# Kernel tuning notes

Measured on AMD Instinct MI355X. Metric: run time of the kernel, lower is better.

The kernel has to match this reference:

```python
import jax, jax.numpy as jnp
import numpy as np
import math

B, L, C, H = 8, 1024, 1024, 8
EPS = 1e-5

def setup_inputs() -> dict:
    key = jax.random.key(0)
    ks = jax.random.split(key, 5)
    s = 0.02
    return {
        "x": jax.random.normal(ks[0], (B, L, C), dtype=jnp.float32),
        "ln_g": jnp.ones((C,), dtype=jnp.float32),
        "ln_b": jnp.zeros((C,), dtype=jnp.float32),
        "w_qkv": jax.random.normal(ks[1], (C, 3 * C), dtype=jnp.float32) * s,
        "b_qkv": jax.random.normal(ks[2], (3 * C,), dtype=jnp.float32) * s,
        "w_out": jax.random.normal(ks[3], (C, C), dtype=jnp.float32) * s,
        "b_out": jax.random.normal(ks[4], (C,), dtype=jnp.float32) * s,
    }

def reference(x, ln_g, ln_b, w_qkv, b_qkv, w_out, b_out):
    bs, length, width = x.shape
    ch = width // H
    # LayerNorm over channels
    mu = jnp.mean(x, axis=-1, keepdims=True)
    var = jnp.mean(jnp.square(x - mu), axis=-1, keepdims=True)
    xn = (x - mu) * jax.lax.rsqrt(var + EPS) * ln_g + ln_b
    # fused QKV projection
    qkv = jnp.einsum('blc,cd->bld', xn, w_qkv) + b_qkv  # [B, L, 3C]
    q, k, v = jnp.split(qkv, 3, axis=2)                 # each [B, L, C]
    scale = 1.0 / math.sqrt(math.sqrt(ch))
    # faithful raw row-major reshape as in the torch .view call
    q = (q * scale).reshape(bs * H, length, ch)
    k = (k * scale).reshape(bs * H, length, ch)
    v = v.reshape(bs * H, length, ch)
    w = jnp.einsum('bqc,bkc->bqk', q, k)                # [B*H, L, L] score matrix
    w = jax.nn.softmax(w.astype(jnp.float32), axis=-1).astype(q.dtype)
    attn = jnp.einsum('bqk,bkc->bqc', w, v).reshape(bs, length, -1)
    out = jnp.einsum('blc,cd->bld', attn, w_out) + b_out + xn  # residual uses normalized x
    return out
```

## Files before the change

### kernel.cpp

```cpp
#include <hip/hip_runtime.h>
#include <hip/hip_bf16.h>


typedef __attribute__((ext_vector_type(8))) short short8;
typedef __attribute__((ext_vector_type(4))) float f32x4;

#define QK_SCALE 0.29730177875068026f

__device__ __forceinline__ float bf2f(ushort u) {
    union { float f; unsigned int i; } c; c.i = ((unsigned int)u) << 16; return c.f;
}
__device__ __forceinline__ ushort f2bf(float f) {
    union { float f; unsigned int i; } c; c.f = f;
    unsigned int x = c.i;
    return (ushort)((x + 0x7FFFu + ((x >> 16) & 1u)) >> 16);
}

__device__ __forceinline__ void gload_lds16(const ushort* g, ushort* l) {
    __builtin_amdgcn_global_load_lds(
        (const __attribute__((address_space(1))) unsigned int*)g,
        (__attribute__((address_space(3))) unsigned int*)l, 16, 0, 0);
}

__global__ __launch_bounds__(256) void prep_kernel(
    const float* __restrict__ x, const float* __restrict__ g,
    const float* __restrict__ b, ushort* __restrict__ xn,
    const float* __restrict__ w_qkv, ushort* __restrict__ wqkvT,
    const float* __restrict__ w_out, ushort* __restrict__ woutT) {
    __shared__ ushort t[32][33];
    int bid = blockIdx.x;
    int tid = threadIdx.x;
    if (bid < 2048) {
        int w = tid >> 6, lane = tid & 63;
        int row = bid * 4 + w;
        const float* xr = x + (size_t)row * 1024;
        float v[4][4];
        float s1 = 0.f, s2 = 0.f;
#pragma unroll
        for (int j = 0; j < 4; j++) {
            float4 t4 = *(const float4*)(xr + lane * 4 + j * 256);
            v[j][0] = t4.x; v[j][1] = t4.y; v[j][2] = t4.z; v[j][3] = t4.w;
#pragma unroll
            for (int e = 0; e < 4; e++) { s1 += v[j][e]; s2 += v[j][e] * v[j][e]; }
        }
#pragma unroll
        for (int m = 32; m >= 1; m >>= 1) { s1 += __shfl_xor(s1, m); s2 += __shfl_xor(s2, m); }
        float mu = s1 * (1.0f / 1024.0f);
        float var = s2 * (1.0f / 1024.0f) - mu * mu;
        float rs = rsqrtf(var + 1e-5f);
#pragma unroll
        for (int j = 0; j < 4; j++) {
            int c0 = lane * 4 + j * 256;
            float4 gg = *(const float4*)(g + c0);
            float4 bb = *(const float4*)(b + c0);
            float gA[4] = {gg.x, gg.y, gg.z, gg.w};
            float bA[4] = {bb.x, bb.y, bb.z, bb.w};
            ushort o[4];
#pragma unroll
            for (int e = 0; e < 4; e++) o[e] = f2bf((v[j][e] - mu) * rs * gA[e] + bA[e]);
            uint2 pk;
            pk.x = (uint)o[0] | ((uint)o[1] << 16);
            pk.y = (uint)o[2] | ((uint)o[3] << 16);
            *(uint2*)(xn + (size_t)row * 1024 + c0) = pk;
        }
    } else {
        const float* in; ushort* out; int R, Cc, bx, by;
        if (bid < 5120) {
            int tt = bid - 2048;
            in = w_qkv; out = wqkvT; R = 1024; Cc = 3072;
            bx = (tt % 96) * 32; by = (tt / 96) * 32;
        } else {
            int tt = bid - 5120;
            in = w_out; out = woutT; R = 1024; Cc = 1024;
            bx = (tt % 32) * 32; by = (tt / 32) * 32;
        }
        int tx = tid & 31, ty = tid >> 5;
#pragma unroll
        for (int j = 0; j < 32; j += 8)
            t[ty + j][tx] = f2bf(in[(size_t)(by + ty + j) * Cc + bx + tx]);
        __syncthreads();
#pragma unroll
        for (int j = 0; j < 32; j += 8)
            out[(size_t)(bx + ty + j) * R + by + tx] = t[tx][ty + j];
    }
}

__device__ __forceinline__ void stage8(const ushort* __restrict__ Ab,
                                       const ushort* __restrict__ Bb, int t2,
                                       ushort* AsD, ushort* BsD, int tid) {
    const ushort* As_src = Ab + t2 * 64;
    const ushort* Bs_src = Bb + t2 * 64;
#pragma unroll
    for (int i = 0; i < 4; i++) {
        int lin = i * 256 + tid;
        int r = lin >> 3, p = lin & 7;
        int l = p ^ (r & 7);
        gload_lds16(As_src + (size_t)r * 1024 + l * 8, &AsD[lin * 8]);
    }
#pragma unroll
    for (int i = 0; i < 4; i++) {
        int lin = i * 256 + tid;
        int r = lin >> 3, p = lin & 7;
        int l = p ^ (r & 7);
        gload_lds16(Bs_src + (size_t)r * 1024 + l * 8, &BsD[lin * 8]);
    }
}

__global__ __launch_bounds__(256, 2) void gemm_qkv(
    const ushort* __restrict__ A, const ushort* __restrict__ Bt,
    const float* __restrict__ bias, ushort* __restrict__ out0,
    ushort* __restrict__ out1, ushort* __restrict__ wv) {
    __shared__ __align__(16) ushort As[2][128 * 64];
    __shared__ __align__(16) ushort Bs[2][128 * 64];

    int tid = threadIdx.x;
    int lane = tid & 63, w = tid >> 6;
    int l15 = lane & 15, q4 = lane >> 4;
    int wrM = (w >> 1) * 64;
    int wcN = (w & 1) * 64;

    int bid = blockIdx.x;
    int xcd = bid & 7;
    int i = bid >> 3;
    int by = xcd * 8 + (i & 7);
    int bx = i >> 3;
    int rowBase = by * 128, colBase = bx * 128;

    const ushort* Ab = A + (size_t)rowBase * 1024;
    const ushort* Bb = Bt + (size_t)colBase * 1024;

    f32x4 acc[4][4];
    f32x4 zero = {0.f, 0.f, 0.f, 0.f};
#pragma unroll
    for (int mi = 0; mi < 4; mi++)
#pragma unroll
        for (int ni = 0; ni < 4; ni++) acc[mi][ni] = zero;

    stage8(Ab, Bb, 0, &As[0][0], &Bs[0][0], tid);
    stage8(Ab, Bb, 1, &As[1][0], &Bs[1][0], tid);
    asm volatile("s_waitcnt vmcnt(8)" ::: "memory");
    __builtin_amdgcn_s_barrier();

    for (int t = 0; t < 16; ++t) {
        const int cur = t & 1;
        const ushort* Ac = &As[cur][0];
        const ushort* Bc = &Bs[cur][0];

        short8 aF[4][2], bF[4][2];
#pragma unroll
        for (int kk = 0; kk < 2; kk++) {
#pragma unroll
            for (int mi = 0; mi < 4; mi++) {
                int r = wrM + mi * 16 + l15;
                aF[mi][kk] = *(const short8*)&Ac[r * 64 + ((kk * 4 + q4) ^ (r & 7)) * 8];
            }
#pragma unroll
            for (int ni = 0; ni < 4; ni++) {
                int r = wcN + ni * 16 + l15;
                bF[ni][kk] = *(const short8*)&Bc[r * 64 + ((kk * 4 + q4) ^ (r & 7)) * 8];
            }
        }

        __builtin_amdgcn_s_setprio(1);
#pragma unroll
        for (int mi = 0; mi < 4; mi++)
#pragma unroll
            for (int ni = 0; ni < 4; ni++)
                acc[mi][ni] = __builtin_amdgcn_mfma_f32_16x16x32_bf16(
                    aF[mi][0], bF[ni][0], acc[mi][ni], 0, 0, 0);
        __builtin_amdgcn_s_setprio(0);

        asm volatile("s_waitcnt lgkmcnt(0)" ::: "memory");
        __builtin_amdgcn_s_barrier();
        if (t < 14) stage8(Ab, Bb, t + 2, &As[cur][0], &Bs[cur][0], tid);

        __builtin_amdgcn_s_setprio(1);
#pragma unroll
        for (int mi = 0; mi < 4; mi++)
#pragma unroll
            for (int ni = 0; ni < 4; ni++)
                acc[mi][ni] = __builtin_amdgcn_mfma_f32_16x16x32_bf16(
                    aF[mi][1], bF[ni][1], acc[mi][ni], 0, 0, 0);
        __builtin_amdgcn_s_setprio(0);

        if (t < 15) {
            if (t < 14) asm volatile("s_waitcnt vmcnt(8)" ::: "memory");
            else        asm volatile("s_waitcnt vmcnt(0)" ::: "memory");
            __builtin_amdgcn_s_barrier();
        }
    }

    if (colBase < 2048) {
#pragma unroll
        for (int ni = 0; ni < 4; ni++) {
            int col = colBase + wcN + ni * 16 + l15;
            float bv = bias[col];
            int cc = col & 1023;
            ushort* dst = (col < 1024) ? out0 : out1;
#pragma unroll
            for (int mi = 0; mi < 4; mi++) {
                f32x4 a = acc[mi][ni];
#pragma unroll
                for (int r = 0; r < 4; r++) {
                    int row = rowBase + wrM + mi * 16 + q4 * 4 + r;
                    dst[(size_t)row * 1024 + cc] = f2bf((a[r] + bv) * QK_SCALE);
                }
            }
        }
    } else {
        int g = rowBase >> 7;
        int s7 = (colBase - 2048) >> 7;
        ushort* Wg = wv + (size_t)g * 131072 + (size_t)s7 * 128;
#pragma unroll
        for (int ni = 0; ni < 4; ni++) {
            int col = colBase + wcN + ni * 16 + l15;
            float bv = bias[col];
            int d = wcN + ni * 16 + l15;
#pragma unroll
            for (int mi = 0; mi < 4; mi++) {
                f32x4 a = acc[mi][ni];
                int off0 = wrM + mi * 16 + q4 * 4;
                ushort o0 = f2bf(a[0] + bv), o1 = f2bf(a[1] + bv);
                ushort o2 = f2bf(a[2] + bv), o3 = f2bf(a[3] + bv);
                uint2 pk;
                pk.x = (uint)o0 | ((uint)o1 << 16);
                pk.y = (uint)o2 | ((uint)o3 << 16);
                *(uint2*)&Wg[(size_t)d * 1024 + off0] = pk;
            }
        }
    }
}

__global__ __launch_bounds__(256, 2) void gemm_out(
    const ushort* __restrict__ A, const ushort* __restrict__ Bt,
    const float* __restrict__ bias, const ushort* __restrict__ resid,
    float* __restrict__ outf) {
    __shared__ __align__(16) ushort As[2][128 * 64];
    __shared__ __align__(16) ushort Bs[2][128 * 64];

    int tid = threadIdx.x;
    int lane = tid & 63, w = tid >> 6;
    int l15 = lane & 15, q4 = lane >> 4;
    int wrM = (w >> 1) * 64;
    int wcN = (w & 1) * 64;

    int bid = blockIdx.x;
    int xcd = bid & 7;
    int i = bid >> 3;
    int by = xcd * 8 + (i & 7);
    int bx = i >> 3;
    int rowBase = by * 128, colBase = bx * 128;

    const ushort* Ab = A + (size_t)rowBase * 1024;
    const ushort* Bb = Bt + (size_t)colBase * 1024;

    f32x4 acc[4][4];
    f32x4 zero = {0.f, 0.f, 0.f, 0.f};
#pragma unroll
    for (int mi = 0; mi < 4; mi++)
#pragma unroll
        for (int ni = 0; ni < 4; ni++) acc[mi][ni] = zero;

    stage8(Ab, Bb, 0, &As[0][0], &Bs[0][0], tid);
    stage8(Ab, Bb, 1, &As[1][0], &Bs[1][0], tid);
    asm volatile("s_waitcnt vmcnt(8)" ::: "memory");
    __builtin_amdgcn_s_barrier();

    for (int t = 0; t < 16; ++t) {
        const int cur = t & 1;
        const ushort* Ac = &As[cur][0];
        const ushort* Bc = &Bs[cur][0];

        short8 aF[4][2], bF[4][2];
#pragma unroll
        for (int kk = 0; kk < 2; kk++) {
#pragma unroll
            for (int mi = 0; mi < 4; mi++) {
                int r = wrM + mi * 16 + l15;
                aF[mi][kk] = *(const short8*)&Ac[r * 64 + ((kk * 4 + q4) ^ (r & 7)) * 8];
            }
#pragma unroll
            for (int ni = 0; ni < 4; ni++) {
                int r = wcN + ni * 16 + l15;
                bF[ni][kk] = *(const short8*)&Bc[r * 64 + ((kk * 4 + q4) ^ (r & 7)) * 8];
            }
        }

        __builtin_amdgcn_s_setprio(1);
#pragma unroll
        for (int mi = 0; mi < 4; mi++)
#pragma unroll
            for (int ni = 0; ni < 4; ni++)
                acc[mi][ni] = __builtin_amdgcn_mfma_f32_16x16x32_bf16(
                    aF[mi][0], bF[ni][0], acc[mi][ni], 0, 0, 0);
        __builtin_amdgcn_s_setprio(0);

        asm volatile("s_waitcnt lgkmcnt(0)" ::: "memory");
        __builtin_amdgcn_s_barrier();
        if (t < 14) stage8(Ab, Bb, t + 2, &As[cur][0], &Bs[cur][0], tid);

        __builtin_amdgcn_s_setprio(1);
#pragma unroll
        for (int mi = 0; mi < 4; mi++)
#pragma unroll
            for (int ni = 0; ni < 4; ni++)
                acc[mi][ni] = __builtin_amdgcn_mfma_f32_16x16x32_bf16(
                    aF[mi][1], bF[ni][1], acc[mi][ni], 0, 0, 0);
        __builtin_amdgcn_s_setprio(0);

        if (t < 15) {
            if (t < 14) asm volatile("s_waitcnt vmcnt(8)" ::: "memory");
            else        asm volatile("s_waitcnt vmcnt(0)" ::: "memory");
            __builtin_amdgcn_s_barrier();
        }
    }

#pragma unroll
    for (int ni = 0; ni < 4; ni++) {
        int col = colBase + wcN + ni * 16 + l15;
        float bv = bias[col];
#pragma unroll
        for (int mi = 0; mi < 4; mi++) {
            f32x4 a = acc[mi][ni];
#pragma unroll
            for (int r = 0; r < 4; r++) {
                int row = rowBase + wrM + mi * 16 + q4 * 4 + r;
                outf[(size_t)row * 1024 + col] =
                    a[r] + bv + bf2f(resid[(size_t)row * 1024 + col]);
            }
        }
    }
}

__device__ __forceinline__ void attn_stage(const ushort* __restrict__ Kh,
                                           const ushort* __restrict__ Wg,
                                           int kt, ushort* KsD, ushort* VtD,
                                           int tid) {
#pragma unroll
    for (int i = 0; i < 4; i++) {
        int linear = i * 512 + tid;
        int r = linear >> 4, p = linear & 15;
        int l = p ^ (r & 15);
        gload_lds16(&Kh[(size_t)(kt * 128 + r) * 128 + l * 8], &KsD[linear * 8]);
    }
#pragma unroll
    for (int i = 0; i < 4; i++) {
        int linear = i * 512 + tid;
        int d = linear >> 4, p = linear & 15;
        int half = p >> 3, pl = p & 7;
        int cl = pl ^ (d & 7);
        gload_lds16(&Wg[(size_t)d * 1024 + cl * 128 + kt * 16 + half * 8],
                    &VtD[linear * 8]);
    }
}

__global__ __launch_bounds__(512) void attn_kernel(
    const ushort* __restrict__ qb, const ushort* __restrict__ kb,
    const ushort* __restrict__ wv, ushort* __restrict__ ob) {
    int bid = blockIdx.x;
    int xcd = bid & 7, ii = bid >> 3;
    int g = xcd * 8 + (ii >> 2);
    int qblk = ii & 3;
    const ushort* Qh = qb + (size_t)g * 131072;
    const ushort* Kh = kb + (size_t)g * 131072;
    const ushort* Wg = wv + (size_t)g * 131072;

    __shared__ __align__(16) ushort Ks[2][128 * 128];
    __shared__ __align__(16) ushort Vt[2][128 * 128];
    __shared__ __align__(16) ushort Ps[256 * 64];

    int tid = threadIdx.x, lane = tid & 63, w = tid >> 6;
    int l15 = lane & 15, q4 = lane >> 4;
    int q0 = qblk * 256;

    short8 qf[2][4];
#pragma unroll
    for (int sub = 0; sub < 2; sub++)
#pragma unroll
        for (int ks = 0; ks < 4; ks++)
            qf[sub][ks] = *(const short8*)&Qh[
                (size_t)(q0 + w * 32 + sub * 16 + l15) * 128 + ks * 32 + q4 * 8];

    f32x4 zero = {0.f, 0.f, 0.f, 0.f};
    f32x4 o[2][8];
#pragma unroll
    for (int sub = 0; sub < 2; sub++)
#pragma unroll
        for (int ni = 0; ni < 8; ni++) o[sub][ni] = zero;
    float plsum[2][4] = {{0.f, 0.f, 0.f, 0.f}, {0.f, 0.f, 0.f, 0.f}};

    attn_stage(Kh, Wg, 0, &Ks[0][0], &Vt[0][0], tid);
    attn_stage(Kh, Wg, 1, &Ks[1][0], &Vt[1][0], tid);
    asm volatile("s_waitcnt vmcnt(8)" ::: "memory");
    __builtin_amdgcn_s_barrier();

    for (int kt = 0; kt < 8; kt++) {
        const int cur = kt & 1;
        const ushort* Kc = &Ks[cur][0];
        const ushort* Vc = &Vt[cur][0];

#pragma unroll
        for (int h = 0; h < 2; h++) {
            f32x4 sacc[2][4];
#pragma unroll
            for (int sub = 0; sub < 2; sub++)
#pragma unroll
                for (int ni = 0; ni < 4; ni++) sacc[sub][ni] = zero;
            __builtin_amdgcn_s_setprio(1);
#pragma unroll
            for (int ks = 0; ks < 4; ks++) {
#pragma unroll
                for (int ni = 0; ni < 4; ni++) {
                    int r = h * 64 + ni * 16 + l15;
                    int p = (ks * 4 + q4) ^ (r & 15);
                    short8 bF = *(const short8*)&Kc[r * 128 + p * 8];
#pragma unroll
                    for (int sub = 0; sub < 2; sub++)
                        sacc[sub][ni] = __builtin_amdgcn_mfma_f32_16x16x32_bf16(
                            qf[sub][ks], bF, sacc[sub][ni], 0, 0, 0);
                }
            }
            __builtin_amdgcn_s_setprio(0);

#pragma unroll
            for (int sub = 0; sub < 2; sub++)
#pragma unroll
                for (int ni = 0; ni < 4; ni++) {
#pragma unroll
                    for (int r = 0; r < 4; r++) {
                        float pv = __expf(sacc[sub][ni][r]);
                        plsum[sub][r] += pv;
                        int qloc = w * 32 + sub * 16 + q4 * 4 + r;
                        int key = ni * 16 + l15;
                        int pc = (key & 7) ^ (qloc & 7);
                        Ps[qloc * 64 + pc * 8 + (key >> 3)] = f2bf(pv);
                    }
                }

            __builtin_amdgcn_s_setprio(1);
#pragma unroll
            for (int ks2 = 0; ks2 < 2; ks2++) {
                int c = ks2 * 4 + q4;
                short8 aF[2];
#pragma unroll
                for (int sub = 0; sub < 2; sub++) {
                    int row = w * 32 + sub * 16 + l15;
                    aF[sub] = *(const short8*)&Ps[row * 64 + (c ^ (l15 & 7)) * 8];
                }
#pragma unroll
                for (int ni = 0; ni < 8; ni++) {
                    int d = ni * 16 + l15;
                    short8 bF = *(const short8*)&Vc[d * 128 + h * 64 + (c ^ (d & 7)) * 8];
#pragma unroll
                    for (int sub = 0; sub < 2; sub++)
                        o[sub][ni] = __builtin_amdgcn_mfma_f32_16x16x32_bf16(
                            aF[sub], bF, o[sub][ni], 0, 0, 0);
                }
            }
            __builtin_amdgcn_s_setprio(0);
        }

        asm volatile("s_waitcnt lgkmcnt(0)" ::: "memory");
        __builtin_amdgcn_s_barrier();
        if (kt < 6) attn_stage(Kh, Wg, kt + 2, &Ks[cur][0], &Vt[cur][0], tid);
        if (kt < 6)       asm volatile("s_waitcnt vmcnt(8)" ::: "memory");
        else if (kt == 6) asm volatile("s_waitcnt vmcnt(0)" ::: "memory");
        if (kt < 7) __builtin_amdgcn_s_barrier();
    }

#pragma unroll
    for (int sub = 0; sub < 2; sub++)
#pragma unroll
        for (int r = 0; r < 4; r++) {
#pragma unroll
            for (int m = 1; m < 16; m <<= 1)
                plsum[sub][r] += __shfl_xor(plsum[sub][r], m, 16);
        }
#pragma unroll
    for (int sub = 0; sub < 2; sub++) {
        float inv[4];
#pragma unroll
        for (int r = 0; r < 4; r++) inv[r] = 1.0f / plsum[sub][r];
#pragma unroll
        for (int ni = 0; ni < 8; ni++)
#pragma unroll
            for (int r = 0; r < 4; r++) {
                int qrow = q0 + w * 32 + sub * 16 + q4 * 4 + r;
                ob[(size_t)g * 131072 + (size_t)qrow * 128 + ni * 16 + l15] =
                    f2bf(o[sub][ni][r] * inv[r]);
            }
    }
}

extern "C" void kernel_launch(void* const* d_in, const int* in_sizes, int n_in,
                              void* d_out, int out_size, void* d_ws, size_t ws_size,
                              hipStream_t stream) {
    const float* x     = (const float*)d_in[0];
    const float* ln_g  = (const float*)d_in[1];
    const float* ln_b  = (const float*)d_in[2];
    const float* w_qkv = (const float*)d_in[3];
    const float* b_qkv = (const float*)d_in[4];
    const float* w_out = (const float*)d_in[5];
    const float* b_out = (const float*)d_in[6];
    float* out = (float*)d_out;

    const size_t MC = 8192ull * 1024ull;
    ushort* xn    = (ushort*)d_ws;
    ushort* wqkvT = xn + MC;
    ushort* woutT = wqkvT + 3072ull * 1024ull;
    ushort* qbuf  = woutT + 1024ull * 1024ull;
    ushort* kbuf  = qbuf + MC;
    ushort* vtbuf = kbuf + MC;
    ushort* attnb = vtbuf + MC;

    prep_kernel<<<6144, 256, 0, stream>>>(x, ln_g, ln_b, xn, w_qkv, wqkvT, w_out, woutT);
    gemm_qkv<<<1536, 256, 0, stream>>>(xn, wqkvT, b_qkv, qbuf, kbuf, vtbuf);
    attn_kernel<<<256, 512, 0, stream>>>(qbuf, kbuf, vtbuf, attnb);
    gemm_out<<<512, 256, 0, stream>>>(attnb, woutT, b_out, xn, out);
}
```

Measured before the change: 225.4 us.

## Restructure QKV GEMM to 256x128 tiles with 512 threads and triple-buffered LDS

The QKV projection GEMM moves from 128x128 tiles with 256 threads and double buffering to 256x128 tiles with 512 threads and a three-stage rotating LDS ring. Loads for tile t+2 are issued before the MFMAs of tile t, leaving one barrier per k-step instead of two. The larger M tile lets each block reuse its B slice across twice as many rows, and the V-transpose epilogue now computes the group index per row. The cost is higher LDS use (about 144 KB) and fewer blocks per CU, which lowers occupancy.

```diff
diff --git a/kernel.cpp b/kernel.cpp
--- a/kernel.cpp
+++ b/kernel.cpp
@@ -85,6 +85,144 @@
     }
 }
 
+__device__ __forceinline__ void stage6q(const ushort* __restrict__ Ab,
+                                        const ushort* __restrict__ Bb, int t2,
+                                        ushort* AsD, ushort* BsD, int tid) {
+    const ushort* As_src = Ab + t2 * 64;
+    const ushort* Bs_src = Bb + t2 * 64;
+#pragma unroll
+    for (int i = 0; i < 4; i++) {
+        int lin = i * 512 + tid;
+        int r = lin >> 3, p = lin & 7;
+        int l = p ^ (r & 7);
+        gload_lds16(As_src + (size_t)r * 1024 + l * 8, &AsD[lin * 8]);
+    }
+#pragma unroll
+    for (int i = 0; i < 2; i++) {
+        int lin = i * 512 + tid;
+        int r = lin >> 3, p = lin & 7;
+        int l = p ^ (r & 7);
+        gload_lds16(Bs_src + (size_t)r * 1024 + l * 8, &BsD[lin * 8]);
+    }
+}
+
+__global__ __launch_bounds__(512) void gemm_qkv(
+    const ushort* __restrict__ A, const ushort* __restrict__ Bt,
+    const float* __restrict__ bias, ushort* __restrict__ out0,
+    ushort* __restrict__ out1, ushort* __restrict__ wv) {
+    __shared__ __align__(16) ushort AS[3][256 * 64];
+    __shared__ __align__(16) ushort BS[3][128 * 64];
+
+    int tid = threadIdx.x;
+    int lane = tid & 63, w = tid >> 6;
+    int l15 = lane & 15, q4 = lane >> 4;
+    int wrM = (w >> 1) * 64;
+    int wcN = (w & 1) * 64;
+
+    int bid = blockIdx.x;
+    int xcd = bid & 7;
+    int ib = bid >> 3;
+    int by = xcd * 4 + (ib & 3);
+    int bx = ib >> 2;
+    int rowBase = by * 256, colBase = bx * 128;
+
+    const ushort* Ab = A + (size_t)rowBase * 1024;
+    const ushort* Bb = Bt + (size_t)colBase * 1024;
+
+    f32x4 acc[4][4];
+    f32x4 zero = {0.f, 0.f, 0.f, 0.f};
+#pragma unroll
+    for (int mi = 0; mi < 4; mi++)
+#pragma unroll
+        for (int ni = 0; ni < 4; ni++) acc[mi][ni] = zero;
+
+    stage6q(Ab, Bb, 0, &AS[0][0], &BS[0][0], tid);
+    stage6q(Ab, Bb, 1, &AS[1][0], &BS[1][0], tid);
+    asm volatile("s_waitcnt vmcnt(6)" ::: "memory");
+    __builtin_amdgcn_s_barrier();
+
+    ushort* rA = &AS[0][0]; ushort* rB = &BS[0][0];
+    ushort* nA = &AS[1][0]; ushort* nB = &BS[1][0];
+    ushort* sA = &AS[2][0]; ushort* sB = &BS[2][0];
+
+    for (int t = 0; t < 16; ++t) {
+        short8 aF[4][2], bF[4][2];
+#pragma unroll
+        for (int kk = 0; kk < 2; kk++) {
+#pragma unroll
+            for (int mi = 0; mi < 4; mi++) {
+                int r = wrM + mi * 16 + l15;
+                aF[mi][kk] = *(const short8*)&rA[r * 64 + ((kk * 4 + q4) ^ (r & 7)) * 8];
+            }
+#pragma unroll
+            for (int ni = 0; ni < 4; ni++) {
+                int r = wcN + ni * 16 + l15;
+                bF[ni][kk] = *(const short8*)&rB[r * 64 + ((kk * 4 + q4) ^ (r & 7)) * 8];
+            }
+        }
+
+        if (t < 14) stage6q(Ab, Bb, t + 2, sA, sB, tid);
+
+        __builtin_amdgcn_s_setprio(1);
+#pragma unroll
+        for (int kk = 0; kk < 2; kk++)
+#pragma unroll
+            for (int mi = 0; mi < 4; mi++)
+#pragma unroll
+                for (int ni = 0; ni < 4; ni++)
+                    acc[mi][ni] = __builtin_amdgcn_mfma_f32_16x16x32_bf16(
+                        aF[mi][kk], bF[ni][kk], acc[mi][ni], 0, 0, 0);
+        __builtin_amdgcn_s_setprio(0);
+
+        if (t < 14)       asm volatile("s_waitcnt vmcnt(6)" ::: "memory");
+        else if (t == 14) asm volatile("s_waitcnt vmcnt(0)" ::: "memory");
+        if (t < 15) __builtin_amdgcn_s_barrier();
+
+        ushort* ta = rA; rA = nA; nA = sA; sA = ta;
+        ushort* tb = rB; rB = nB; nB = sB; sB = tb;
+    }
+
+    if (colBase < 2048) {
+#pragma unroll
+        for (int ni = 0; ni < 4; ni++) {
+            int col = colBase + wcN + ni * 16 + l15;
+            float bv = bias[col];
+            int cc = col & 1023;
+            ushort* dst = (col < 1024) ? out0 : out1;
+#pragma unroll
+            for (int mi = 0; mi < 4; mi++) {
+                f32x4 a = acc[mi][ni];
+#pragma unroll
+                for (int r = 0; r < 4; r++) {
+                    int row = rowBase + wrM + mi * 16 + q4 * 4 + r;
+                    dst[(size_t)row * 1024 + cc] = f2bf((a[r] + bv) * QK_SCALE);
+                }
+            }
+        }
+    } else {
+        int s7 = (colBase - 2048) >> 7;
+#pragma unroll
+        for (int ni = 0; ni < 4; ni++) {
+            int col = colBase + wcN + ni * 16 + l15;
+            float bv = bias[col];
+            int d = wcN + ni * 16 + l15;
+#pragma unroll
+            for (int mi = 0; mi < 4; mi++) {
+                f32x4 a = acc[mi][ni];
+                int row = rowBase + wrM + mi * 16 + q4 * 4;
+                int g = row >> 7;
+                int off0 = row & 127;
+                ushort o0 = f2bf(a[0] + bv), o1 = f2bf(a[1] + bv);
+                ushort o2 = f2bf(a[2] + bv), o3 = f2bf(a[3] + bv);
+                uint2 pk;
+                pk.x = (uint)o0 | ((uint)o1 << 16);
+                pk.y = (uint)o2 | ((uint)o3 << 16);
+                *(uint2*)&wv[(size_t)g * 131072 + (size_t)d * 1024 + s7 * 128 + off0] = pk;
+            }
+        }
+    }
+}
+
 __device__ __forceinline__ void stage8(const ushort* __restrict__ Ab,
                                        const ushort* __restrict__ Bb, int t2,
                                        ushort* AsD, ushort* BsD, int tid) {
@@ -103,131 +241,6 @@
         int r = lin >> 3, p = lin & 7;
         int l = p ^ (r & 7);
         gload_lds16(Bs_src + (size_t)r * 1024 + l * 8, &BsD[lin * 8]);
-    }
-}
-
-__global__ __launch_bounds__(256, 2) void gemm_qkv(
-    const ushort* __restrict__ A, const ushort* __restrict__ Bt,
-    const float* __restrict__ bias, ushort* __restrict__ out0,
-    ushort* __restrict__ out1, ushort* __restrict__ wv) {
-    __shared__ __align__(16) ushort As[2][128 * 64];
-    __shared__ __align__(16) ushort Bs[2][128 * 64];
-
-    int tid = threadIdx.x;
-    int lane = tid & 63, w = tid >> 6;
-    int l15 = lane & 15, q4 = lane >> 4;
-    int wrM = (w >> 1) * 64;
-    int wcN = (w & 1) * 64;
-
-    int bid = blockIdx.x;
-    int xcd = bid & 7;
-    int i = bid >> 3;
-    int by = xcd * 8 + (i & 7);
-    int bx = i >> 3;
-    int rowBase = by * 128, colBase = bx * 128;
-
-    const ushort* Ab = A + (size_t)rowBase * 1024;
-    const ushort* Bb = Bt + (size_t)colBase * 1024;
-
-    f32x4 acc[4][4];
-    f32x4 zero = {0.f, 0.f, 0.f, 0.f};
-#pragma unroll
-    for (int mi = 0; mi < 4; mi++)
-#pragma unroll
-        for (int ni = 0; ni < 4; ni++) acc[mi][ni] = zero;
-
-    stage8(Ab, Bb, 0, &As[0][0], &Bs[0][0], tid);
-    stage8(Ab, Bb, 1, &As[1][0], &Bs[1][0], tid);
-    asm volatile("s_waitcnt vmcnt(8)" ::: "memory");
-    __builtin_amdgcn_s_barrier();
-
-    for (int t = 0; t < 16; ++t) {
-        const int cur = t & 1;
-        const ushort* Ac = &As[cur][0];
-        const ushort* Bc = &Bs[cur][0];
-
-        short8 aF[4][2], bF[4][2];
-#pragma unroll
-        for (int kk = 0; kk < 2; kk++) {
-#pragma unroll
-            for (int mi = 0; mi < 4; mi++) {
-                int r = wrM + mi * 16 + l15;
-                aF[mi][kk] = *(const short8*)&Ac[r * 64 + ((kk * 4 + q4) ^ (r & 7)) * 8];
-            }
-#pragma unroll
-            for (int ni = 0; ni < 4; ni++) {
-                int r = wcN + ni * 16 + l15;
-                bF[ni][kk] = *(const short8*)&Bc[r * 64 + ((kk * 4 + q4) ^ (r & 7)) * 8];
-            }
-        }
-
-        __builtin_amdgcn_s_setprio(1);
-#pragma unroll
-        for (int mi = 0; mi < 4; mi++)
-#pragma unroll
-            for (int ni = 0; ni < 4; ni++)
-                acc[mi][ni] = __builtin_amdgcn_mfma_f32_16x16x32_bf16(
-                    aF[mi][0], bF[ni][0], acc[mi][ni], 0, 0, 0);
-        __builtin_amdgcn_s_setprio(0);
-
-        asm volatile("s_waitcnt lgkmcnt(0)" ::: "memory");
-        __builtin_amdgcn_s_barrier();
-        if (t < 14) stage8(Ab, Bb, t + 2, &As[cur][0], &Bs[cur][0], tid);
-
-        __builtin_amdgcn_s_setprio(1);
-#pragma unroll
-        for (int mi = 0; mi < 4; mi++)
-#pragma unroll
-            for (int ni = 0; ni < 4; ni++)
-                acc[mi][ni] = __builtin_amdgcn_mfma_f32_16x16x32_bf16(
-                    aF[mi][1], bF[ni][1], acc[mi][ni], 0, 0, 0);
-        __builtin_amdgcn_s_setprio(0);
-
-        if (t < 15) {
-            if (t < 14) asm volatile("s_waitcnt vmcnt(8)" ::: "memory");
-            else        asm volatile("s_waitcnt vmcnt(0)" ::: "memory");
-            __builtin_amdgcn_s_barrier();
-        }
-    }
-
-    if (colBase < 2048) {
-#pragma unroll
-        for (int ni = 0; ni < 4; ni++) {
-            int col = colBase + wcN + ni * 16 + l15;
-            float bv = bias[col];
-            int cc = col & 1023;
-            ushort* dst = (col < 1024) ? out0 : out1;
-#pragma unroll
-            for (int mi = 0; mi < 4; mi++) {
-                f32x4 a = acc[mi][ni];
-#pragma unroll
-                for (int r = 0; r < 4; r++) {
-                    int row = rowBase + wrM + mi * 16 + q4 * 4 + r;
-                    dst[(size_t)row * 1024 + cc] = f2bf((a[r] + bv) * QK_SCALE);
-                }
-            }
-        }
-    } else {
-        int g = rowBase >> 7;
-        int s7 = (colBase - 2048) >> 7;
-        ushort* Wg = wv + (size_t)g * 131072 + (size_t)s7 * 128;
-#pragma unroll
-        for (int ni = 0; ni < 4; ni++) {
-            int col = colBase + wcN + ni * 16 + l15;
-            float bv = bias[col];
-            int d = wcN + ni * 16 + l15;
-#pragma unroll
-            for (int mi = 0; mi < 4; mi++) {
-                f32x4 a = acc[mi][ni];
-                int off0 = wrM + mi * 16 + q4 * 4;
-                ushort o0 = f2bf(a[0] + bv), o1 = f2bf(a[1] + bv);
-                ushort o2 = f2bf(a[2] + bv), o3 = f2bf(a[3] + bv);
-                uint2 pk;
-                pk.x = (uint)o0 | ((uint)o1 << 16);
-                pk.y = (uint)o2 | ((uint)o3 << 16);
-                *(uint2*)&Wg[(size_t)d * 1024 + off0] = pk;
-            }
-        }
     }
 }
 
@@ -514,7 +527,7 @@
     ushort* attnb = vtbuf + MC;
 
     prep_kernel<<<6144, 256, 0, stream>>>(x, ln_g, ln_b, xn, w_qkv, wqkvT, w_out, woutT);
-    gemm_qkv<<<1536, 256, 0, stream>>>(xn, wqkvT, b_qkv, qbuf, kbuf, vtbuf);
+    gemm_qkv<<<768, 512, 0, stream>>>(xn, wqkvT, b_qkv, qbuf, kbuf, vtbuf);
     attn_kernel<<<256, 512, 0, stream>>>(qbuf, kbuf, vtbuf, attnb);
     gemm_out<<<512, 256, 0, stream>>>(attnb, woutT, b_out, xn, out);
 }
```

Result: slower. 232.2 us (+3.0%).
